# Kernel optimization log

Measured on AMD Instinct MI355X. Metric: run time of the kernel, lower is better.

Reference implementation:

```python
import jax, jax.numpy as jnp
import numpy as np
from jax import lax

SQRT2 = float(np.sqrt(2.0))  # lrelu def_gain
LRELU_SLOPE = 0.2


def setup_inputs() -> dict:
    key = jax.random.key(0)
    ks = jax.random.split(key, 4)
    N, I, O, WD, H = 16, 256, 512, 512, 64
    return {
        "x": jax.random.normal(ks[0], (N, I, H, H), dtype=jnp.float32),
        "w": jax.random.normal(ks[1], (N, WD), dtype=jnp.float32),
        "affine_w": jax.random.normal(ks[2], (I, WD), dtype=jnp.float32),
        "affine_b": jnp.ones((I,), dtype=jnp.float32),
        "weight": jax.random.normal(ks[3], (O, I, 3, 3), dtype=jnp.float32),
        "bias": jnp.zeros((O,), dtype=jnp.float32),
    }


def reference(x, w, affine_w, affine_b, weight, bias):
    N, I, H, W = x.shape
    O, _, kh, kw = weight.shape
    w_dim = affine_w.shape[1]

    # affine (FullyConnectedLayer, weight_gain = 1/sqrt(w_dim))
    styles = w @ (affine_w.T / np.sqrt(w_dim)) + affine_b  # [N, I]

    # modulate + demodulate -> per-sample weights [N, O, I, kh, kw]
    ww = weight[None] * styles[:, None, :, None, None]
    dcoefs = lax.rsqrt(jnp.sum(ww * ww, axis=(2, 3, 4)) + 1e-8)  # [N, O]
    ww = ww * dcoefs[:, :, None, None, None]

    # resample filter: outer([1,3,3,1])/sum, symmetric so flip is a no-op
    f1 = jnp.array([1.0, 3.0, 3.0, 1.0], dtype=x.dtype)
    f1 = f1 / f1.sum()
    f2 = jnp.outer(f1, f1)  # [4, 4]

    # upfirdn2d: pad by padding + (fw-down+1)//2 = 2 per side, depthwise 4x4
    xp = jnp.pad(x, ((0, 0), (0, 0), (2, 2), (2, 2)))
    fk = jnp.broadcast_to(f2[None, None], (I, 1, 4, 4))
    xf = lax.conv_general_dilated(
        xp, fk, window_strides=(1, 1), padding="VALID",
        feature_group_count=I,
        dimension_numbers=("NCHW", "OIHW", "NCHW"))  # [N, I, H+1, W+1]

    # fused grouped conv, stride 2; flip_weight=False -> flip kernel spatially
    wk = ww[:, :, :, ::-1, ::-1].reshape(N * O, I, kh, kw)
    xg = xf.reshape(1, N * I, xf.shape[2], xf.shape[3])
    y = lax.conv_general_dilated(
        xg, wk, window_strides=(2, 2), padding="VALID",
        feature_group_count=N,
        dimension_numbers=("NCHW", "OIHW", "NCHW"))
    y = y.reshape(N, O, y.shape[2], y.shape[3])  # [N, O, H/2, W/2]

    # bias + lrelu, act_gain = sqrt(2), no clamp
    y = y + bias[None, :, None, None]
    y = jnp.where(y >= 0, y, LRELU_SLOPE * y) * SQRT2
    return y
```

## Files before the change

kernel.cpp:

```cpp
#include <hip/hip_runtime.h>
#include <cstdint>
#include <cstddef>


typedef short bf16x8 __attribute__((ext_vector_type(8)));
typedef float f32x4  __attribute__((ext_vector_type(4)));
typedef float f32x16 __attribute__((ext_vector_type(16)));

#define CGSTR 4460544
#define NSTR  278784
#define PLSTR 69696

__device__ __forceinline__ unsigned short f2bf(float f) {
  union { float f; unsigned u; } v; v.f = f;
  unsigned r = (v.u + 0x7FFFu + ((v.u >> 16) & 1u)) >> 16;
  return (unsigned short)r;
}

__device__ __forceinline__ void gload_lds16(const void* g, void* l) {
  __builtin_amdgcn_global_load_lds((const __attribute__((address_space(1))) void*)g,
                                   (__attribute__((address_space(3))) void*)l,
                                   16, 0, 0);
}

__global__ void wtcvt_kernel(const float* __restrict__ wt, const float* __restrict__ w,
                             const float* __restrict__ aw, const float* __restrict__ ab,
                             unsigned short* __restrict__ wtb, float* __restrict__ wsq,
                             float* __restrict__ styles) {
  const int o = blockIdx.x;
  const int i = threadIdx.x;
  const float* p = wt + ((size_t)o * 256 + i) * 9;
  float v[9];
  float s = 0.f;
#pragma unroll
  for (int k = 0; k < 9; ++k) { v[k] = p[k]; s += v[k] * v[k]; }
  wsq[o * 256 + i] = s;
#pragma unroll
  for (int tap = 0; tap < 9; ++tap)
    wtb[((size_t)tap * 512 + o) * 256 + i] = f2bf(v[8 - tap]);
  if (o < 16) {
    const float4* wr = (const float4*)(w + (size_t)o * 512);
    const float4* ar = (const float4*)(aw + (size_t)i * 512);
    float acc = 0.f;
#pragma unroll 4
    for (int k = 0; k < 128; ++k) {
      float4 a = wr[k], c = ar[k];
      acc += a.x * c.x + a.y * c.y + a.z * c.z + a.w * c.w;
    }
    styles[o * 256 + i] = acc * 0.04419417382415922f + ab[i];
  }
}

__global__ void dcoefs_kernel(const float* __restrict__ wsq, const float* __restrict__ styles,
                              float* __restrict__ dcoefs) {
  __shared__ float st2[256];
  const int n = blockIdx.x;
  const int t = threadIdx.x;
  if (t < 256) { float s = styles[n * 256 + t]; st2[t] = s * s; }
  __syncthreads();
  const float4* wr = (const float4*)(wsq + (size_t)t * 256);
  const float4* sr = (const float4*)st2;
  float acc = 0.f;
#pragma unroll 4
  for (int k = 0; k < 64; ++k) {
    float4 a = wr[k], c = sr[k];
    acc += a.x * c.x + a.y * c.y + a.z * c.z + a.w * c.w;
  }
  dcoefs[n * 512 + t] = 1.0f / sqrtf(acc + 1e-8f);
}

__global__ __launch_bounds__(256, 4) void blur_kernel(const float* __restrict__ x,
                                                      const float* __restrict__ styles,
                                                      unsigned short* __restrict__ xfp) {
  __shared__ unsigned short shls[2][64][68];
  const int b = blockIdx.x;
  const int n = b >> 5;
  const int rem = b & 31;
  const int rg = rem >> 2;
  const int cg = rem & 3;
  const int tid = threadIdx.x;
  const int ch = tid >> 2;
  const int s4 = tid & 3;
  const int col0 = s4 * 16;
  const float* xin = x + ((size_t)(n * 256 + cg * 64 + ch) << 12);
  const float sv = styles[n * 256 + cg * 64 + ch];
  const float F0s = 0.125f * sv, F1s = 0.375f * sv;
  const float F0 = 0.125f, F1 = 0.375f;
  const int ybase = rg * 8;
  const int ylim = (rg == 7) ? 9 : 8;
  const size_t obase = (size_t)(cg * 16 + n) * 4 * PLSTR;

  float4 rA[4], rB[4], rC[4], rD[4], rN[4];
  auto load4 = [&](int row, float4* dst) {
    if ((unsigned)row < 64u) {
      const float4* p = (const float4*)(xin + row * 64 + col0);
      dst[0] = p[0]; dst[1] = p[1]; dst[2] = p[2]; dst[3] = p[3];
    } else {
      const float4 z = {0.f, 0.f, 0.f, 0.f};
      dst[0] = z; dst[1] = z; dst[2] = z; dst[3] = z;
    }
  };
  load4(ybase - 2, rA); load4(ybase - 1, rB); load4(ybase, rC); load4(ybase + 1, rD);

#pragma unroll 1
  for (int yy = 0; yy < ylim; ++yy) {
    const int y = ybase + yy;
    load4(y + 2, rN);
    float ve[20];
#pragma unroll
    for (int q = 0; q < 4; ++q) {
      ve[2 + q * 4 + 0] = F0s * rA[q].x + F1s * rB[q].x + F1s * rC[q].x + F0s * rD[q].x;
      ve[2 + q * 4 + 1] = F0s * rA[q].y + F1s * rB[q].y + F1s * rC[q].y + F0s * rD[q].y;
      ve[2 + q * 4 + 2] = F0s * rA[q].z + F1s * rB[q].z + F1s * rC[q].z + F0s * rD[q].z;
      ve[2 + q * 4 + 3] = F0s * rA[q].w + F1s * rB[q].w + F1s * rC[q].w + F0s * rD[q].w;
    }
    float vm2 = __shfl_up(ve[16], 1);
    float vm1 = __shfl_up(ve[17], 1);
    float vp1 = __shfl_down(ve[2], 1);
    if (s4 == 0) { vm2 = 0.f; vm1 = 0.f; }
    if (s4 == 3) vp1 = 0.f;
    ve[0] = vm2; ve[1] = vm1; ve[18] = vp1; ve[19] = 0.f;
    unsigned short hv[17];
#pragma unroll
    for (int pl = 0; pl < 17; ++pl)
      hv[pl] = f2bf(F0 * ve[pl] + F1 * ve[pl + 1] + F1 * ve[pl + 2] + F0 * ve[pl + 3]);
    unsigned short (*sh)[68] = shls[yy & 1];
    unsigned* dst32 = (unsigned*)&sh[ch][col0];
#pragma unroll
    for (int q = 0; q < 8; ++q)
      dst32[q] = (unsigned)hv[2 * q] | ((unsigned)hv[2 * q + 1] << 16);
    if (s4 == 3) sh[ch][64] = hv[16];
    __syncthreads();
    const int ph = y & 1, r = y >> 1;
#pragma unroll 1
    for (int sI = tid; sI < 520; sI += 256) {
      const int p = sI >> 3, j = sI & 7;
      union { bf16x8 vv; unsigned short u[8]; } pk;
#pragma unroll
      for (int k = 0; k < 8; ++k) pk.u[k] = sh[j * 8 + k][p];
      const int pw = p & 1, cc = p >> 1;
      const size_t off = obase + (size_t)(ph * 2 + pw) * PLSTR + (r * 33 + cc) * 64 + j * 8;
      *(bf16x8*)(xfp + off) = pk.vv;
    }
#pragma unroll
    for (int q = 0; q < 4; ++q) { rA[q] = rB[q]; rB[q] = rC[q]; rC[q] = rD[q]; rD[q] = rN[q]; }
  }
}

__global__ __launch_bounds__(256) void conv_kernel(
    const unsigned short* __restrict__ wtb,
    const unsigned short* __restrict__ xfp,
    const float* __restrict__ dcoefs,
    const float* __restrict__ bias,
    float* __restrict__ out) {
  __shared__ unsigned short As0[8192], Bs0[8192];
  __shared__ unsigned short As1[8192], Bs1[8192];
  const int idx = blockIdx.x;
  const int om = idx >> 7;
  const int g = idx & 127;
  const int pt = g >> 4;
  const int n = g & 15;
  const int o0 = om << 7;
  const int oh0 = pt << 2;
  const int tid = threadIdx.x;
  const int lane = tid & 63;
  const int wv = tid >> 6;
  const int wm = wv >> 1;
  const int wp = wv & 1;
  const int l31 = lane & 31;
  const int half = lane >> 5;

  f32x16 acc[2][2];
#pragma unroll
  for (int i = 0; i < 2; ++i)
#pragma unroll
    for (int j = 0; j < 2; ++j)
#pragma unroll
      for (int e = 0; e < 16; ++e) acc[i][j][e] = 0.f;

  const int rowbase = wv * 32 + (lane >> 3);
  const int glog8 = (((lane & 7) ^ ((lane >> 3) & 7))) * 8;
  int aoffj[4], boffj[4];
#pragma unroll
  for (int j = 0; j < 4; ++j) {
    const int r = rowbase + j * 8;
    aoffj[j] = (o0 + r) * 256 + glog8;
    boffj[j] = ((oh0 + (r >> 5)) * 33 + (r & 31)) * 64 + glog8;
  }
  const size_t nB = (size_t)n * NSTR;
  int gi[4];
#pragma unroll
  for (int c = 0; c < 4; ++c) gi[c] = (c * 2 + half) ^ (lane & 7);

  auto stage = [&](int kt, unsigned short* As, unsigned short* Bs) {
    const int tap = kt >> 2, pair = kt & 3;
    const int kh = (tap * 11) >> 5;
    const int kw = tap - kh * 3;
    const int ph = kh & 1, dr = kh >> 1;
    const int pw = kw & 1, dc = kw >> 1;
    const unsigned short* At = wtb + tap * 131072 + pair * 64;
    const unsigned short* Bt = xfp + (size_t)pair * CGSTR + nB +
                               (size_t)(ph * 2 + pw) * PLSTR + (dr * 33 + dc) * 64;
#pragma unroll
    for (int j = 0; j < 4; ++j) {
      gload_lds16(At + aoffj[j], As + (wv * 256 + j * 64) * 8);
      gload_lds16(Bt + boffj[j], Bs + (wv * 256 + j * 64) * 8);
    }
  };
  auto compute = [&](const unsigned short* As, const unsigned short* Bs) {
    const bf16x8* A8 = (const bf16x8*)As;
    const bf16x8* B8 = (const bf16x8*)Bs;
#pragma unroll
    for (int c = 0; c < 4; ++c) {
      bf16x8 af[2], bfv[2];
#pragma unroll
      for (int t = 0; t < 2; ++t) {
        af[t]  = A8[(wm * 64 + t * 32 + l31) * 8 + gi[c]];
        bfv[t] = B8[(wp * 64 + t * 32 + l31) * 8 + gi[c]];
      }
#pragma unroll
      for (int mt = 0; mt < 2; ++mt)
#pragma unroll
        for (int nt = 0; nt < 2; ++nt)
          acc[mt][nt] = __builtin_amdgcn_mfma_f32_32x32x16_bf16(af[mt], bfv[nt], acc[mt][nt], 0, 0, 0);
    }
  };

  stage(0, As0, Bs0);
#pragma unroll 1
  for (int kt = 0; kt < 36; kt += 2) {
    __syncthreads();
    stage(kt + 1, As1, Bs1);
    compute(As0, Bs0);
    __syncthreads();
    if (kt + 2 < 36) stage(kt + 2, As0, Bs0);
    compute(As1, Bs1);
  }

  f32x4 dc4[2][4], bi4[2][4];
#pragma unroll
  for (int mt = 0; mt < 2; ++mt)
#pragma unroll
    for (int i = 0; i < 4; ++i) {
      const int ob = o0 + wm * 64 + mt * 32 + i * 8 + half * 4;
      dc4[mt][i] = *(const f32x4*)(dcoefs + n * 512 + ob);
      bi4[mt][i] = *(const f32x4*)(bias + ob);
    }
#pragma unroll
  for (int mt = 0; mt < 2; ++mt) {
#pragma unroll
    for (int nt = 0; nt < 2; ++nt) {
      const int oh = oh0 + wp * 2 + nt;
      const int ow = l31;
#pragma unroll
      for (int i = 0; i < 4; ++i) {
#pragma unroll
        for (int r = 0; r < 4; ++r) {
          const int o = o0 + wm * 64 + mt * 32 + i * 8 + half * 4 + r;
          float v = acc[mt][nt][i * 4 + r] * dc4[mt][i][r] + bi4[mt][i][r];
          v = (v >= 0.f ? v : 0.2f * v) * 1.41421356237309515f;
          out[(((size_t)n * 512 + o) * 32 + oh) * 32 + ow] = v;
        }
      }
    }
  }
}

extern "C" void kernel_launch(void* const* d_in, const int* in_sizes, int n_in,
                              void* d_out, int out_size, void* d_ws, size_t ws_size,
                              hipStream_t stream) {
  const float* x  = (const float*)d_in[0];
  const float* w  = (const float*)d_in[1];
  const float* aw = (const float*)d_in[2];
  const float* ab = (const float*)d_in[3];
  const float* wt = (const float*)d_in[4];
  const float* bs = (const float*)d_in[5];
  float* out = (float*)d_out;

  char* ws = (char*)d_ws;
  float* styles        = (float*)(ws);
  float* dcoefs        = (float*)(ws + 16384);
  float* wsq           = (float*)(ws + 49152);
  unsigned short* wtb  = (unsigned short*)(ws + 573440);
  unsigned short* xfp  = (unsigned short*)(ws + 2932736);

  wtcvt_kernel <<<dim3(512),  dim3(256), 0, stream>>>(wt, w, aw, ab, wtb, wsq, styles);
  dcoefs_kernel<<<dim3(16),   dim3(512), 0, stream>>>(wsq, styles, dcoefs);
  blur_kernel  <<<dim3(512),  dim3(256), 0, stream>>>(x, styles, xfp);
  conv_kernel  <<<dim3(512),  dim3(256), 0, stream>>>(wtb, xfp, dcoefs, bs, out);
}
```

Baseline: 200.7 us.

## Fuse dcoefs into blur launch, transpose blur LDS layout, rotate MFMA k-chunks

The dcoefs computation now runs as 16 extra blocks appended to the blur kernel's grid, which removes one kernel launch and its serialization gap. The blur kernel's shared-memory tile is stored transposed, position-major with a padded stride, so each output bf16x8 vector comes from a single 16-byte LDS read instead of eight scattered 2-byte reads. The conv kernel rotates the k-chunk order per wave to spread LDS bank accesses. The cost is a larger LDS footprint in blur and scattered 2-byte LDS writes on the store side.

```diff
diff --git a/kernel.cpp b/kernel.cpp
--- a/kernel.cpp
+++ b/kernel.cpp
@@ -10,6 +10,7 @@
 #define CGSTR 4460544
 #define NSTR  278784
 #define PLSTR 69696
+#define PSTR  136
 
 __device__ __forceinline__ unsigned short f2bf(float f) {
   union { float f; unsigned u; } v; v.f = f;
@@ -51,34 +52,40 @@
   }
 }
 
-__global__ void dcoefs_kernel(const float* __restrict__ wsq, const float* __restrict__ styles,
-                              float* __restrict__ dcoefs) {
-  __shared__ float st2[256];
-  const int n = blockIdx.x;
-  const int t = threadIdx.x;
-  if (t < 256) { float s = styles[n * 256 + t]; st2[t] = s * s; }
-  __syncthreads();
-  const float4* wr = (const float4*)(wsq + (size_t)t * 256);
-  const float4* sr = (const float4*)st2;
-  float acc = 0.f;
-#pragma unroll 4
-  for (int k = 0; k < 64; ++k) {
-    float4 a = wr[k], c = sr[k];
-    acc += a.x * c.x + a.y * c.y + a.z * c.z + a.w * c.w;
-  }
-  dcoefs[n * 512 + t] = 1.0f / sqrtf(acc + 1e-8f);
-}
-
 __global__ __launch_bounds__(256, 4) void blur_kernel(const float* __restrict__ x,
                                                       const float* __restrict__ styles,
-                                                      unsigned short* __restrict__ xfp) {
-  __shared__ unsigned short shls[2][64][68];
+                                                      const float* __restrict__ wsq,
+                                                      unsigned short* __restrict__ xfp,
+                                                      float* __restrict__ dcoefs) {
+  __shared__ unsigned short shp[2][65 * PSTR];
+  __shared__ float st2[256];
   const int b = blockIdx.x;
+  const int tid = threadIdx.x;
+
+  if (b >= 512) {
+    const int n = b - 512;
+    { float sv = styles[n * 256 + tid]; st2[tid] = sv * sv; }
+    __syncthreads();
+    const float4* sr = (const float4*)st2;
+#pragma unroll 1
+    for (int oo = 0; oo < 2; ++oo) {
+      const int o = oo * 256 + tid;
+      const float4* wr = (const float4*)(wsq + (size_t)o * 256);
+      float acc = 0.f;
+#pragma unroll 4
+      for (int k = 0; k < 64; ++k) {
+        float4 a = wr[k], c = sr[k];
+        acc += a.x * c.x + a.y * c.y + a.z * c.z + a.w * c.w;
+      }
+      dcoefs[n * 512 + o] = 1.0f / sqrtf(acc + 1e-8f);
+    }
+    return;
+  }
+
   const int n = b >> 5;
   const int rem = b & 31;
   const int rg = rem >> 2;
   const int cg = rem & 3;
-  const int tid = threadIdx.x;
   const int ch = tid >> 2;
   const int s4 = tid & 3;
   const int col0 = s4 * 16;
@@ -124,23 +131,22 @@
 #pragma unroll
     for (int pl = 0; pl < 17; ++pl)
       hv[pl] = f2bf(F0 * ve[pl] + F1 * ve[pl + 1] + F1 * ve[pl + 2] + F0 * ve[pl + 3]);
-    unsigned short (*sh)[68] = shls[yy & 1];
-    unsigned* dst32 = (unsigned*)&sh[ch][col0];
-#pragma unroll
-    for (int q = 0; q < 8; ++q)
-      dst32[q] = (unsigned)hv[2 * q] | ((unsigned)hv[2 * q + 1] << 16);
-    if (s4 == 3) sh[ch][64] = hv[16];
+    unsigned short* sh = shp[yy & 1];
+#pragma unroll
+    for (int k = 0; k < 16; ++k) {
+      const int pl = (k + s4 * 4) & 15;
+      sh[(col0 + pl) * PSTR + ch] = hv[pl];
+    }
+    if (s4 == 3) sh[64 * PSTR + ch] = hv[16];
     __syncthreads();
     const int ph = y & 1, r = y >> 1;
 #pragma unroll 1
     for (int sI = tid; sI < 520; sI += 256) {
       const int p = sI >> 3, j = sI & 7;
-      union { bf16x8 vv; unsigned short u[8]; } pk;
-#pragma unroll
-      for (int k = 0; k < 8; ++k) pk.u[k] = sh[j * 8 + k][p];
+      bf16x8 vv = *(const bf16x8*)&sh[p * PSTR + j * 8];
       const int pw = p & 1, cc = p >> 1;
       const size_t off = obase + (size_t)(ph * 2 + pw) * PLSTR + (r * 33 + cc) * 64 + j * 8;
-      *(bf16x8*)(xfp + off) = pk.vv;
+      *(bf16x8*)(xfp + off) = vv;
     }
 #pragma unroll
     for (int q = 0; q < 4; ++q) { rA[q] = rB[q]; rB[q] = rC[q]; rC[q] = rD[q]; rD[q] = rN[q]; }
@@ -211,12 +217,13 @@
     const bf16x8* A8 = (const bf16x8*)As;
     const bf16x8* B8 = (const bf16x8*)Bs;
 #pragma unroll
-    for (int c = 0; c < 4; ++c) {
+    for (int c0 = 0; c0 < 4; ++c0) {
+      const int cc = (c0 + wv) & 3;
       bf16x8 af[2], bfv[2];
 #pragma unroll
       for (int t = 0; t < 2; ++t) {
-        af[t]  = A8[(wm * 64 + t * 32 + l31) * 8 + gi[c]];
-        bfv[t] = B8[(wp * 64 + t * 32 + l31) * 8 + gi[c]];
+        af[t]  = A8[(wm * 64 + t * 32 + l31) * 8 + gi[cc]];
+        bfv[t] = B8[(wp * 64 + t * 32 + l31) * 8 + gi[cc]];
       }
 #pragma unroll
       for (int mt = 0; mt < 2; ++mt)
@@ -285,7 +292,6 @@
   unsigned short* xfp  = (unsigned short*)(ws + 2932736);
 
   wtcvt_kernel <<<dim3(512),  dim3(256), 0, stream>>>(wt, w, aw, ab, wtb, wsq, styles);
-  dcoefs_kernel<<<dim3(16),   dim3(512), 0, stream>>>(wsq, styles, dcoefs);
-  blur_kernel  <<<dim3(512),  dim3(256), 0, stream>>>(x, styles, xfp);
+  blur_kernel  <<<dim3(528),  dim3(256), 0, stream>>>(x, styles, wsq, xfp, dcoefs);
   conv_kernel  <<<dim3(512),  dim3(256), 0, stream>>>(wtb, xfp, dcoefs, bs, out);
 }
```

Result: slower. 246.8 us (+23.0%).
